# Performance work log

Hardware: AMD Instinct MI355X
Metric: run time of the kernel (lower is better)

Reference implementation:

```python
import jax, jax.numpy as jnp
import numpy as np

B, P, N = 64, 100, 1000
D, H, QD = 128, 8, 16
NUM_PATCHES = 196
NTOT = N + NUM_PATCHES
SQRT_D = float(np.sqrt(D))   # sqrt_embedding_dim
CLIP = 10.0                  # logit_clipping


def setup_inputs() -> dict:
    key = jax.random.key(0)
    ks = jax.random.split(key, 10)
    return {
        "encoded_last_node": jax.random.normal(ks[0], (B, P, D), jnp.float32),
        "ninf_mask": jnp.zeros((B, P, N), jnp.float32),
        "q_first": jax.random.normal(ks[1], (B, H, P, QD), jnp.float32),
        "k": jax.random.normal(ks[2], (B, H, NTOT, QD), jnp.float32),
        "v": jax.random.normal(ks[3], (B, H, NTOT, QD), jnp.float32),
        "single_head_key": jax.random.normal(ks[4], (B, D, N), jnp.float32),
        "Wq_last": jax.random.normal(ks[5], (D, H * QD), jnp.float32) * 0.05,
        "mh_combine": jax.random.normal(ks[6], (H * QD, D), jnp.float32) * 0.05,
        "edge_bias": jax.random.normal(ks[7], (B, N, N), jnp.float32) * 0.1,
        "current_node": jax.random.randint(ks[8], (B, P), 0, N, jnp.int64),
        "num_patches": NUM_PATCHES,
    }


def reference(encoded_last_node, ninf_mask, q_first, k, v, single_head_key,
              Wq_last, mh_combine, edge_bias, current_node, num_patches):
    b, p, _ = encoded_last_node.shape
    h, qd = q_first.shape[1], q_first.shape[3]

    # q_last = reshape_by_heads(F.linear(x, Wq_last_para))  -> [B,H,P,qd]
    q_last = (encoded_last_node @ Wq_last.T).reshape(b, p, h, qd).transpose(0, 2, 1, 3)
    q = q_first + q_last

    # multi-head attention with mask extended by zero columns for patch tokens
    mask_full = jnp.pad(ninf_mask, ((0, 0), (0, 0), (0, num_patches)))  # [B,P,Ntot]
    score = jnp.einsum('bhpd,bhnd->bhpn', q, k) / jnp.sqrt(jnp.float32(qd))
    weights = jax.nn.softmax(score + mask_full[:, None, :, :], axis=-1)
    out = jnp.einsum('bhpn,bhnd->bhpd', weights, v)
    out_concat = out.transpose(0, 2, 1, 3).reshape(b, p, h * qd)  # [B,P,D]

    mh_atten_out = out_concat @ mh_combine.T                       # [B,P,D]

    # pointer-style single-head score with tanh clipping
    score2 = jnp.einsum('bpd,bdn->bpn', mh_atten_out, single_head_key)
    score_clipped = CLIP * jnp.tanh(score2 / SQRT_D)

    # gather edge bias row for current node: bias[b,p,n] = edge_bias[b, current_node[b,p], n]
    bias_row = jnp.take_along_axis(edge_bias, current_node[:, :, None], axis=1)
    probs = jax.nn.softmax(score_clipped + bias_row + ninf_mask, axis=-1)
    return probs
```

## Files before the change

### kernel.cpp

```cpp
#include <hip/hip_runtime.h>
#include <hip/hip_bf16.h>
#include <math.h>

#define BB 64
#define PP 100
#define NN 1000
#define DD 128
#define HH 8
#define QDQ 16
#define NTOT 1196
#define HALFK 598
#define CH 128
#define QROWS 16
#define LOG2E 1.44269504088896f
#define EXP2(x) __builtin_amdgcn_exp2f(x)

typedef float f2 __attribute__((ext_vector_type(2)));
static __device__ __forceinline__ f2 splat2(float v) { f2 r; r.x = v; r.y = v; return r; }
#define PKFMA(a, b, c) __builtin_elementwise_fma((a), (b), (c))

__global__ __launch_bounds__(256) void k_prep(const float* __restrict__ x,
                                              const float* __restrict__ Wq,
                                              const float* __restrict__ qf,
                                              float* __restrict__ qout,
                                              const float* __restrict__ mask,
                                              __hip_bfloat16* __restrict__ mt) {
  __shared__ float sw[128 * 65];
  __shared__ float xs[QROWS * DD];
  int tid = threadIdx.x;

  if (blockIdx.x < 400) {
    int row0 = blockIdx.x * QROWS;
    for (int i = tid; i < QROWS * DD / 4; i += 256)
      ((float4*)xs)[i] = ((const float4*)(x + (size_t)row0 * DD))[i];

    int j = tid & 127, rr = tid >> 7;
    float acc[8];
#pragma unroll
    for (int i = 0; i < 8; ++i) acc[i] = 0.f;

    for (int half = 0; half < 2; ++half) {
      __syncthreads();
      for (int idx = tid; idx < 128 * 64; idx += 256) {
        int jj = idx >> 6, dl = idx & 63;
        sw[jj * 65 + dl] = Wq[jj * DD + half * 64 + dl];
      }
      __syncthreads();
#pragma unroll
      for (int ri = 0; ri < 8; ++ri) {
        int r = 2 * ri + rr;
        float a = acc[ri];
#pragma unroll 16
        for (int dl = 0; dl < 64; ++dl)
          a += xs[r * DD + half * 64 + dl] * sw[j * 65 + dl];
        acc[ri] = a;
      }
    }
#pragma unroll
    for (int ri = 0; ri < 8; ++ri) {
      int bp = row0 + 2 * ri + rr;
      int b = bp / PP, p = bp % PP;
      int h = j >> 4, qd = j & 15;
      size_t qi = ((size_t)(b * HH + h) * PP + p) * QDQ + qd;
      qout[qi] = acc[ri] + qf[qi];
    }
  } else {
    float (*tile)[65] = (float(*)[65])sw;
    int t = blockIdx.x - 400;
    int b = t / 38, rem = t % 38;
    int nt = rem % 19, pt = rem / 19;
    int tx = tid & 63, ty = tid >> 6;
    int n0 = nt * 64, p0 = pt * 64;
#pragma unroll
    for (int r = ty; r < 64; r += 4) {
      int p = p0 + r, n = n0 + tx;
      tile[r][tx] = (p < PP && n < NN) ? mask[((size_t)b * PP + p) * NN + n] * LOG2E - 20.f
                                       : -20.f;
    }
    __syncthreads();
#pragma unroll
    for (int r = ty; r < 64; r += 4) {
      int n = n0 + r, p = p0 + tx;
      int pp = ((p & 63) << 1) | (p >> 6);
      if (n < NTOT)
        mt[((size_t)b * NTOT + n) * 128 + pp] = __float2bfloat16(tile[tx][r]);
    }
  }
}

#define QKDOT(qv, K0, K1, K2, K3) \
  (qv[0] * K0.x + qv[1] * K0.y + qv[2] * K0.z + qv[3] * K0.w \
 + qv[4] * K1.x + qv[5] * K1.y + qv[6] * K1.z + qv[7] * K1.w \
 + qv[8] * K2.x + qv[9] * K2.y + qv[10] * K2.z + qv[11] * K2.w \
 + qv[12] * K3.x + qv[13] * K3.y + qv[14] * K3.z + qv[15] * K3.w)

#define PVADD(av, wt, V0, V1, V2, V3) { \
  av[0] += (wt) * V0.x;  av[1] += (wt) * V0.y;  av[2] += (wt) * V0.z;  av[3] += (wt) * V0.w; \
  av[4] += (wt) * V1.x;  av[5] += (wt) * V1.y;  av[6] += (wt) * V1.z;  av[7] += (wt) * V1.w; \
  av[8] += (wt) * V2.x;  av[9] += (wt) * V2.y;  av[10] += (wt) * V2.z; av[11] += (wt) * V2.w; \
  av[12] += (wt) * V3.x; av[13] += (wt) * V3.y; av[14] += (wt) * V3.z; av[15] += (wt) * V3.w; }

__global__ __launch_bounds__(512) void k_mha(const float* __restrict__ kk,
                                             const float* __restrict__ vv,
                                             const float* __restrict__ qws,
                                             const unsigned int* __restrict__ mt32,
                                             float* __restrict__ part) {
  int bid = blockIdx.x;
  int swz = (bid & 7) * 128 + (bid >> 3);
  int bh = swz >> 1, half = swz & 1;
  int b = bh >> 3;
  int tid = threadIdx.x;
  int w = tid >> 6;
  int lane = tid & 63;
  int p2 = lane + 64;
  int pc2 = p2 < PP ? p2 : PP - 1;

  __shared__ __align__(16) float smem_f[8192];
  float4* s4 = (float4*)smem_f;

  float q1[QDQ], q2[QDQ];
  const float sc0 = 0.25f * LOG2E;
  {
    const float* qrow1 = qws + ((size_t)bh * PP + lane) * QDQ;
    const float* qrow2 = qws + ((size_t)bh * PP + pc2) * QDQ;
#pragma unroll
    for (int jj = 0; jj < QDQ; jj += 4) {
      float4 a4 = *(const float4*)(qrow1 + jj);
      q1[jj] = a4.x * sc0; q1[jj + 1] = a4.y * sc0;
      q1[jj + 2] = a4.z * sc0; q1[jj + 3] = a4.w * sc0;
      float4 b4 = *(const float4*)(qrow2 + jj);
      q2[jj] = b4.x * sc0; q2[jj + 1] = b4.y * sc0;
      q2[jj + 2] = b4.z * sc0; q2[jj + 3] = b4.w * sc0;
    }
  }

  float acc1[QDQ], acc2[QDQ];
#pragma unroll
  for (int jj = 0; jj < QDQ; ++jj) { acc1[jj] = 0.f; acc2[jj] = 0.f; }
  float l1 = 0.f, l2 = 0.f;

  const float4* kg4 = (const float4*)(kk + (size_t)bh * NTOT * QDQ);
  const float4* vg4 = (const float4*)(vv + (size_t)bh * NTOT * QDQ);
  int key0 = half * HALFK;
  int gbase = key0 * 4;
  int lim = NTOT * 4 - 1;

  float4 rk, rv;
  { int gi = gbase + tid; gi = gi < lim ? gi : lim; rk = kg4[gi]; rv = vg4[gi]; }

  int cur = 0;
  for (int c = 0; c < 5; ++c) {
    int base = c * CH;
    int L = HALFK - base; if (L > CH) L = CH;
    __syncthreads();
    s4[cur * 1024 + tid] = rk;
    s4[cur * 1024 + 512 + tid] = rv;
    __syncthreads();
    if (c < 4) {
      int gi = gbase + (c + 1) * 512 + tid; gi = gi < lim ? gi : lim;
      rk = kg4[gi]; rv = vg4[gi];
    }
    const unsigned int* mrow = mt32 + ((size_t)b * NTOT + key0 + base) * 64;
    int kb = cur * 1024, vb = cur * 1024 + 512;

    unsigned int nmm = mrow[w * 64 + lane];
    for (int i = w; i < L; i += 8) {
      unsigned int mm = nmm;
      int inx = i + 8; inx = inx < L ? inx : i;
      nmm = mrow[inx * 64 + lane];

      float4 k0 = s4[kb + i * 4 + 0], k1 = s4[kb + i * 4 + 1];
      float4 k2 = s4[kb + i * 4 + 2], k3 = s4[kb + i * 4 + 3];
      float s1 = QKDOT(q1, k0, k1, k2, k3);
      float s2 = QKDOT(q2, k0, k1, k2, k3);
      float w1 = EXP2(s1 + __uint_as_float(mm << 16));
      float w2 = EXP2(s2 + __uint_as_float(mm & 0xffff0000u));
      l1 += w1; l2 += w2;
      float4 v0 = s4[vb + i * 4 + 0], v1 = s4[vb + i * 4 + 1];
      float4 v2 = s4[vb + i * 4 + 2], v3 = s4[vb + i * 4 + 3];
      PVADD(acc1, w1, v0, v1, v2, v3)
      PVADD(acc2, w2, v0, v1, v2, v3)
    }
    cur ^= 1;
  }

  __syncthreads();
  if (w < 4) {
    float* r = smem_f + ((size_t)w * PP + lane) * 17;
#pragma unroll
    for (int jj = 0; jj < QDQ; ++jj) r[jj] = acc1[jj];
    r[16] = l1;
    if (p2 < PP) {
      float* r2 = smem_f + ((size_t)w * PP + p2) * 17;
#pragma unroll
      for (int jj = 0; jj < QDQ; ++jj) r2[jj] = acc2[jj];
      r2[16] = l2;
    }
  }
  __syncthreads();
  if (w >= 4) {
    float* r = smem_f + ((size_t)(w - 4) * PP + lane) * 17;
#pragma unroll
    for (int jj = 0; jj < QDQ; ++jj) r[jj] += acc1[jj];
    r[16] += l1;
    if (p2 < PP) {
      float* r2 = smem_f + ((size_t)(w - 4) * PP + p2) * 17;
#pragma unroll
      for (int jj = 0; jj < QDQ; ++jj) r2[jj] += acc2[jj];
      r2[16] += l2;
    }
  }
  __syncthreads();
  for (int idx = tid; idx < PP * 17; idx += 512) {
    int pp2 = idx / 17, e = idx % 17;
    float vsum = smem_f[(0 * PP + pp2) * 17 + e] + smem_f[(1 * PP + pp2) * 17 + e]
               + smem_f[(2 * PP + pp2) * 17 + e] + smem_f[(3 * PP + pp2) * 17 + e];
    part[((size_t)swz * PP + pp2) * 17 + e] = vsum;
  }
}

__global__ __launch_bounds__(256) void k_combine(const float* __restrict__ part,
                                                 const float* __restrict__ MC,
                                                 float* __restrict__ mh) {
  __shared__ float sw[128 * 65];
  __shared__ float oc[QROWS * DD];
  int tid = threadIdx.x;
  int row0 = blockIdx.x * QROWS;

  for (int i = tid; i < QROWS * DD; i += 256) {
    int r = i >> 7, t = i & 127;
    int bp = row0 + r, b = bp / PP, p = bp % PP;
    int qd = t & 15, h = t >> 4;
    int bh = b * HH + h;
    const float* r0 = part + (((size_t)(bh * 2 + 0)) * PP + p) * 17;
    const float* r1 = part + (((size_t)(bh * 2 + 1)) * PP + p) * 17;
    float A = r0[qd] + r1[qd];
    float L = r0[16] + r1[16];
    oc[i] = A / L;
  }

  int j = tid & 127, rr = tid >> 7;
  float acc[8];
#pragma unroll
  for (int i = 0; i < 8; ++i) acc[i] = 0.f;

  for (int half = 0; half < 2; ++half) {
    __syncthreads();
    for (int idx = tid; idx < 128 * 64; idx += 256) {
      int jj = idx >> 6, dl = idx & 63;
      sw[jj * 65 + dl] = MC[jj * DD + half * 64 + dl];
    }
    __syncthreads();
#pragma unroll
    for (int ri = 0; ri < 8; ++ri) {
      int r = 2 * ri + rr;
      float a = acc[ri];
#pragma unroll 16
      for (int dl = 0; dl < 64; ++dl)
        a += oc[r * DD + half * 64 + dl] * sw[j * 65 + dl];
      acc[ri] = a;
    }
  }
#pragma unroll
  for (int ri = 0; ri < 8; ++ri) {
    int bp = row0 + 2 * ri + rr;
    mh[(size_t)bp * DD + j] = acc[ri];
  }
}

__global__ __launch_bounds__(256) void k_score2(const float* __restrict__ mh,
                                                const float* __restrict__ shk,
                                                float* __restrict__ sc) {
  int bid = blockIdx.x;
  int swz = (bid & 7) * 128 + (bid >> 3);
  int b = swz >> 4, nt = swz & 15;
  int tid = threadIdx.x; int nl = tid & 31, pg = tid >> 5;
  __shared__ float A[PP * 132];
  for (int idx = tid; idx < PP * DD; idx += 256)
    A[(idx >> 7) * 132 + (idx & 127)] = mh[(size_t)b * PP * DD + idx];
  __syncthreads();

  int na = nt * 64 + nl, nb2 = na + 32;
  int nca = na < NN ? na : NN - 1, ncb = nb2 < NN ? nb2 : NN - 1;
  const float* S = shk + (size_t)b * DD * NN;
  f2 accv[13];
#pragma unroll
  for (int i = 0; i < 13; ++i) accv[i] = splat2(0.f);

  for (int d = 0; d < DD; d += 4) {
    f2 s0, s1, s2, s3;
    s0.x = S[(size_t)(d + 0) * NN + nca]; s0.y = S[(size_t)(d + 0) * NN + ncb];
    s1.x = S[(size_t)(d + 1) * NN + nca]; s1.y = S[(size_t)(d + 1) * NN + ncb];
    s2.x = S[(size_t)(d + 2) * NN + nca]; s2.y = S[(size_t)(d + 2) * NN + ncb];
    s3.x = S[(size_t)(d + 3) * NN + nca]; s3.y = S[(size_t)(d + 3) * NN + ncb];
#pragma unroll
    for (int i = 0; i < 13; ++i) {
      int p = pg + (i << 3);
      if (p < PP) {
        const float4 a4 = *(const float4*)&A[p * 132 + d];
        accv[i] = PKFMA(splat2(a4.x), s0, accv[i]);
        accv[i] = PKFMA(splat2(a4.y), s1, accv[i]);
        accv[i] = PKFMA(splat2(a4.z), s2, accv[i]);
        accv[i] = PKFMA(splat2(a4.w), s3, accv[i]);
      }
    }
  }
#pragma unroll
  for (int i = 0; i < 13; ++i) {
    int p = pg + (i << 3);
    if (p < PP) {
      size_t base = ((size_t)b * PP + p) * NN;
      if (na < NN) sc[base + na] = accv[i].x;
      if (nb2 < NN) sc[base + nb2] = accv[i].y;
    }
  }
}

__global__ __launch_bounds__(256) void k_finsm(const float* __restrict__ sc,
                                               const float* __restrict__ eb,
                                               const int* __restrict__ cn,
                                               const float* __restrict__ mask,
                                               float* __restrict__ out) {
  int bid = blockIdx.x;
  int bp = (bid & 7) * 800 + (bid >> 3);
  int b = bp / PP;
  int t = threadIdx.x;
  int node = cn[bp];
  const float* scp = sc + (size_t)bp * NN;
  const float* ebp = eb + ((size_t)b * NN + node) * NN;
  const float* mp = mask + (size_t)bp * NN;
  const float inv_sqrtD = 0.08838834764831845f;

  float vals[4];
  float s = 0.f;
#pragma unroll
  for (int i = 0; i < 4; ++i) {
    int n = t + (i << 8);
    if (n < NN) {
      float z = scp[n] * inv_sqrtD;
      float e = EXP2(2.f * LOG2E * z);
      float th10 = 10.f - 20.f * __builtin_amdgcn_rcpf(e + 1.f);
      float lg = th10 + ebp[n] + mp[n];
      float e2 = EXP2(lg * LOG2E);
      vals[i] = e2;
      s += e2;
    } else {
      vals[i] = 0.f;
    }
  }
#pragma unroll
  for (int off = 32; off; off >>= 1) s += __shfl_xor(s, off);
  __shared__ float red[4];
  int w = t >> 6, lane = t & 63;
  if (lane == 0) red[w] = s;
  __syncthreads();
  s = (red[0] + red[1]) + (red[2] + red[3]);
  float inv = 1.f / s;
#pragma unroll
  for (int i = 0; i < 4; ++i) {
    int n = t + (i << 8);
    if (n < NN) out[(size_t)bp * NN + n] = vals[i] * inv;
  }
}

extern "C" void kernel_launch(void* const* d_in, const int* in_sizes, int n_in,
                              void* d_out, int out_size, void* d_ws, size_t ws_size,
                              hipStream_t stream) {
  const float* x    = (const float*)d_in[0];
  const float* mask = (const float*)d_in[1];
  const float* qf   = (const float*)d_in[2];
  const float* kk   = (const float*)d_in[3];
  const float* vv   = (const float*)d_in[4];
  const float* shk  = (const float*)d_in[5];
  const float* Wq   = (const float*)d_in[6];
  const float* MC   = (const float*)d_in[7];
  const float* eb   = (const float*)d_in[8];
  const int*   cn   = (const int*)d_in[9];

  float* out = (float*)d_out;
  float* ws = (float*)d_ws;
  float* q_ws = ws;
  float* part = ws + 819200;
  float* mh   = ws + 2560000;
  float* reg  = ws + 3379200;
  __hip_bfloat16* mt = (__hip_bfloat16*)reg;
  float* sc   = reg;

  hipLaunchKernelGGL(k_prep, dim3(2832), dim3(256), 0, stream, x, Wq, qf, q_ws, mask, mt);
  hipLaunchKernelGGL(k_mha, dim3(1024), dim3(512), 0, stream, kk, vv, q_ws,
                     (const unsigned int*)mt, part);
  hipLaunchKernelGGL(k_combine, dim3(400), dim3(256), 0, stream, part, MC, mh);
  hipLaunchKernelGGL(k_score2, dim3(1024), dim3(256), 0, stream, mh, shk, sc);
  hipLaunchKernelGGL(k_finsm, dim3(6400), dim3(256), 0, stream, sc, eb, cn, mask, out);
}
```

Baseline: 219.9 us.

## Move attention QK and PV onto bf16 MFMA with split-precision hi/lo operands

Replaces the scalar FP32 dot-product attention loop in k_mha with 32x32x16 bf16 MFMA instructions. Q, K, V and the softmax weights are each split into a bf16 high part and a bf16 residual, and three MFMAs per product recover near-FP32 accuracy. The mask is pre-laid out per query row, padded to 1280 keys, and loaded directly as the MFMA accumulator initializer. The block size drops to 256 threads and k_prep gets more blocks for the new mask layout. This trades scalar VALU FMA work for matrix-core throughput, at the cost of extra conversion and shuffle work, LDS transposes, and a larger mask buffer.

```diff
diff --git a/kernel.cpp b/kernel.cpp
--- a/kernel.cpp
+++ b/kernel.cpp
@@ -1,5 +1,4 @@
 #include <hip/hip_runtime.h>
-#include <hip/hip_bf16.h>
 #include <math.h>
 
 #define BB 64
@@ -9,22 +8,31 @@
 #define HH 8
 #define QDQ 16
 #define NTOT 1196
-#define HALFK 598
-#define CH 128
 #define QROWS 16
 #define LOG2E 1.44269504088896f
 #define EXP2(x) __builtin_amdgcn_exp2f(x)
 
 typedef float f2 __attribute__((ext_vector_type(2)));
+typedef short s8v __attribute__((ext_vector_type(8)));
+typedef float f16v __attribute__((ext_vector_type(16)));
+
 static __device__ __forceinline__ f2 splat2(float v) { f2 r; r.x = v; r.y = v; return r; }
 #define PKFMA(a, b, c) __builtin_elementwise_fma((a), (b), (c))
+
+static __device__ __forceinline__ unsigned pkhi(float a, float b) {
+  return (__float_as_uint(a) >> 16) | (__float_as_uint(b) & 0xffff0000u);
+}
+static __device__ __forceinline__ float truncbf(float a) {
+  return __uint_as_float(__float_as_uint(a) & 0xffff0000u);
+}
+#define MFMA32(a, b, c) __builtin_amdgcn_mfma_f32_32x32x16_bf16((a), (b), (c), 0, 0, 0)
 
 __global__ __launch_bounds__(256) void k_prep(const float* __restrict__ x,
                                               const float* __restrict__ Wq,
                                               const float* __restrict__ qf,
                                               float* __restrict__ qout,
                                               const float* __restrict__ mask,
-                                              __hip_bfloat16* __restrict__ mt) {
+                                              unsigned short* __restrict__ m2) {
   __shared__ float sw[128 * 65];
   __shared__ float xs[QROWS * DD];
   int tid = threadIdx.x;
@@ -65,157 +73,198 @@
       qout[qi] = acc[ri] + qf[qi];
     }
   } else {
-    float (*tile)[65] = (float(*)[65])sw;
-    int t = blockIdx.x - 400;
-    int b = t / 38, rem = t % 38;
-    int nt = rem % 19, pt = rem / 19;
-    int tx = tid & 63, ty = tid >> 6;
-    int n0 = nt * 64, p0 = pt * 64;
-#pragma unroll
-    for (int r = ty; r < 64; r += 4) {
-      int p = p0 + r, n = n0 + tx;
-      tile[r][tx] = (p < PP && n < NN) ? mask[((size_t)b * PP + p) * NN + n] * LOG2E - 20.f
-                                       : -20.f;
-    }
-    __syncthreads();
-#pragma unroll
-    for (int r = ty; r < 64; r += 4) {
-      int n = n0 + r, p = p0 + tx;
-      int pp = ((p & 63) << 1) | (p >> 6);
-      if (n < NTOT)
-        mt[((size_t)b * NTOT + n) * 128 + pp] = __float2bfloat16(tile[tx][r]);
-    }
-  }
-}
-
-#define QKDOT(qv, K0, K1, K2, K3) \
-  (qv[0] * K0.x + qv[1] * K0.y + qv[2] * K0.z + qv[3] * K0.w \
- + qv[4] * K1.x + qv[5] * K1.y + qv[6] * K1.z + qv[7] * K1.w \
- + qv[8] * K2.x + qv[9] * K2.y + qv[10] * K2.z + qv[11] * K2.w \
- + qv[12] * K3.x + qv[13] * K3.y + qv[14] * K3.z + qv[15] * K3.w)
-
-#define PVADD(av, wt, V0, V1, V2, V3) { \
-  av[0] += (wt) * V0.x;  av[1] += (wt) * V0.y;  av[2] += (wt) * V0.z;  av[3] += (wt) * V0.w; \
-  av[4] += (wt) * V1.x;  av[5] += (wt) * V1.y;  av[6] += (wt) * V1.z;  av[7] += (wt) * V1.w; \
-  av[8] += (wt) * V2.x;  av[9] += (wt) * V2.y;  av[10] += (wt) * V2.z; av[11] += (wt) * V2.w; \
-  av[12] += (wt) * V3.x; av[13] += (wt) * V3.y; av[14] += (wt) * V3.z; av[15] += (wt) * V3.w; }
-
-__global__ __launch_bounds__(512) void k_mha(const float* __restrict__ kk,
+    int t2 = blockIdx.x - 400;
+    int b = t2 >> 7, q = t2 & 127;
+    unsigned short* dst = m2 + (size_t)(b * 128 + q) * 1280;
+    const float* srow = mask + ((size_t)b * PP + (q < PP ? q : PP - 1)) * NN;
+    for (int j = tid; j < 1280; j += 256) {
+      int h = j >= 640 ? 1 : 0;
+      int jj = j - h * 640;
+      float val;
+      if (q >= PP || jj >= 598) {
+        val = -1e4f;
+      } else {
+        int n = h * 598 + jj;
+        val = (n < NN) ? srow[n] * LOG2E - 20.f : -20.f;
+      }
+      dst[j] = (unsigned short)(__float_as_uint(val) >> 16);
+    }
+  }
+}
+
+__global__ __launch_bounds__(256) void k_mha(const float* __restrict__ kk,
                                              const float* __restrict__ vv,
                                              const float* __restrict__ qws,
-                                             const unsigned int* __restrict__ mt32,
+                                             const unsigned short* __restrict__ m2,
                                              float* __restrict__ part) {
   int bid = blockIdx.x;
   int swz = (bid & 7) * 128 + (bid >> 3);
   int bh = swz >> 1, half = swz & 1;
   int b = bh >> 3;
   int tid = threadIdx.x;
-  int w = tid >> 6;
-  int lane = tid & 63;
-  int p2 = lane + 64;
-  int pc2 = p2 < PP ? p2 : PP - 1;
-
-  __shared__ __align__(16) float smem_f[8192];
-  float4* s4 = (float4*)smem_f;
-
-  float q1[QDQ], q2[QDQ];
-  const float sc0 = 0.25f * LOG2E;
+  int w = tid >> 6, lane = tid & 63;
+  int L = lane >> 5, ln = lane & 31;
+  bool lo = (L == 0);
+
+  __shared__ __align__(16) char pool[27264];
+  char* KspB = pool;
+  char* VThB = pool + 8192;
+  char* VTlB = pool + 12288;
+  char* QhB  = pool + 16384;
+  char* QlB  = pool + 20480;
+
   {
-    const float* qrow1 = qws + ((size_t)bh * PP + lane) * QDQ;
-    const float* qrow2 = qws + ((size_t)bh * PP + pc2) * QDQ;
-#pragma unroll
-    for (int jj = 0; jj < QDQ; jj += 4) {
-      float4 a4 = *(const float4*)(qrow1 + jj);
-      q1[jj] = a4.x * sc0; q1[jj + 1] = a4.y * sc0;
-      q1[jj + 2] = a4.z * sc0; q1[jj + 3] = a4.w * sc0;
-      float4 b4 = *(const float4*)(qrow2 + jj);
-      q2[jj] = b4.x * sc0; q2[jj + 1] = b4.y * sc0;
-      q2[jj + 2] = b4.z * sc0; q2[jj + 3] = b4.w * sc0;
-    }
-  }
-
-  float acc1[QDQ], acc2[QDQ];
-#pragma unroll
-  for (int jj = 0; jj < QDQ; ++jj) { acc1[jj] = 0.f; acc2[jj] = 0.f; }
-  float l1 = 0.f, l2 = 0.f;
-
-  const float4* kg4 = (const float4*)(kk + (size_t)bh * NTOT * QDQ);
-  const float4* vg4 = (const float4*)(vv + (size_t)bh * NTOT * QDQ);
-  int key0 = half * HALFK;
-  int gbase = key0 * 4;
-  int lim = NTOT * 4 - 1;
-
-  float4 rk, rv;
-  { int gi = gbase + tid; gi = gi < lim ? gi : lim; rk = kg4[gi]; rv = vg4[gi]; }
-
-  int cur = 0;
+    const float* qrow = qws + (size_t)bh * (PP * QDQ);
+    for (int i = tid; i < 128 * 16; i += 256) {
+      int p = i >> 4, qd = i & 15;
+      float v = (p < PP) ? qrow[p * QDQ + qd] * (0.25f * LOG2E) : 0.f;
+      ((unsigned short*)QhB)[i] = (unsigned short)(__float_as_uint(v) >> 16);
+      float rl = v - truncbf(v);
+      ((unsigned short*)QlB)[i] = (unsigned short)(__float_as_uint(rl) >> 16);
+    }
+  }
+
+  const float4* kf4 = (const float4*)kk + (size_t)bh * NTOT * 4;
+  const float4* vf4 = (const float4*)vv + (size_t)bh * NTOT * 4;
+
+  f16v Oacc[4];
+  float lacc[4];
+#pragma unroll
+  for (int qt = 0; qt < 4; ++qt) {
+    lacc[qt] = 0.f;
+#pragma unroll
+    for (int r = 0; r < 16; ++r) Oacc[qt][r] = 0.f;
+  }
+  s8v QhF[4], QlF[4];
+
   for (int c = 0; c < 5; ++c) {
-    int base = c * CH;
-    int L = HALFK - base; if (L > CH) L = CH;
     __syncthreads();
-    s4[cur * 1024 + tid] = rk;
-    s4[cur * 1024 + 512 + tid] = rv;
+#pragma unroll
+    for (int rep = 0; rep < 2; ++rep) {
+      int f = tid + rep * 256;
+      int key_l = f >> 2, qd0 = (f & 3) << 2;
+      int j = c * 128 + key_l;
+      int jc = j < 598 ? j : 597;
+      size_t gidx = (size_t)(half * 598 + jc) * 4 + (qd0 >> 2);
+      float4 k4 = kf4[gidx];
+      unsigned kh01 = pkhi(k4.x, k4.y), kh23 = pkhi(k4.z, k4.w);
+      float r0 = k4.x - truncbf(k4.x), r1 = k4.y - truncbf(k4.y);
+      float r2 = k4.z - truncbf(k4.z), r3 = k4.w - truncbf(k4.w);
+      unsigned kl01 = pkhi(r0, r1), kl23 = pkhi(r2, r3);
+      *(uint2*)(KspB + key_l * 64 + qd0 * 2) = make_uint2(kh01, kh23);
+      *(uint2*)(KspB + key_l * 64 + 32 + qd0 * 2) = make_uint2(kl01, kl23);
+      float4 v4 = vf4[gidx];
+      float ve0 = v4.x, ve1 = v4.y, ve2 = v4.z, ve3 = v4.w;
+      ((unsigned short*)VThB)[(qd0 + 0) * 128 + key_l] = (unsigned short)(__float_as_uint(ve0) >> 16);
+      ((unsigned short*)VThB)[(qd0 + 1) * 128 + key_l] = (unsigned short)(__float_as_uint(ve1) >> 16);
+      ((unsigned short*)VThB)[(qd0 + 2) * 128 + key_l] = (unsigned short)(__float_as_uint(ve2) >> 16);
+      ((unsigned short*)VThB)[(qd0 + 3) * 128 + key_l] = (unsigned short)(__float_as_uint(ve3) >> 16);
+      float w0 = ve0 - truncbf(ve0), w1 = ve1 - truncbf(ve1);
+      float w2 = ve2 - truncbf(ve2), w3 = ve3 - truncbf(ve3);
+      ((unsigned short*)VTlB)[(qd0 + 0) * 128 + key_l] = (unsigned short)(__float_as_uint(w0) >> 16);
+      ((unsigned short*)VTlB)[(qd0 + 1) * 128 + key_l] = (unsigned short)(__float_as_uint(w1) >> 16);
+      ((unsigned short*)VTlB)[(qd0 + 2) * 128 + key_l] = (unsigned short)(__float_as_uint(w2) >> 16);
+      ((unsigned short*)VTlB)[(qd0 + 3) * 128 + key_l] = (unsigned short)(__float_as_uint(w3) >> 16);
+    }
     __syncthreads();
-    if (c < 4) {
-      int gi = gbase + (c + 1) * 512 + tid; gi = gi < lim ? gi : lim;
-      rk = kg4[gi]; rv = vg4[gi];
-    }
-    const unsigned int* mrow = mt32 + ((size_t)b * NTOT + key0 + base) * 64;
-    int kb = cur * 1024, vb = cur * 1024 + 512;
-
-    unsigned int nmm = mrow[w * 64 + lane];
-    for (int i = w; i < L; i += 8) {
-      unsigned int mm = nmm;
-      int inx = i + 8; inx = inx < L ? inx : i;
-      nmm = mrow[inx * 64 + lane];
-
-      float4 k0 = s4[kb + i * 4 + 0], k1 = s4[kb + i * 4 + 1];
-      float4 k2 = s4[kb + i * 4 + 2], k3 = s4[kb + i * 4 + 3];
-      float s1 = QKDOT(q1, k0, k1, k2, k3);
-      float s2 = QKDOT(q2, k0, k1, k2, k3);
-      float w1 = EXP2(s1 + __uint_as_float(mm << 16));
-      float w2 = EXP2(s2 + __uint_as_float(mm & 0xffff0000u));
-      l1 += w1; l2 += w2;
-      float4 v0 = s4[vb + i * 4 + 0], v1 = s4[vb + i * 4 + 1];
-      float4 v2 = s4[vb + i * 4 + 2], v3 = s4[vb + i * 4 + 3];
-      PVADD(acc1, w1, v0, v1, v2, v3)
-      PVADD(acc2, w2, v0, v1, v2, v3)
-    }
-    cur ^= 1;
-  }
+    if (c == 0) {
+#pragma unroll
+      for (int qt = 0; qt < 4; ++qt) {
+        int qr = qt * 32 + ln;
+        QhF[qt] = *(const s8v*)(QhB + qr * 32 + L * 16);
+        QlF[qt] = *(const s8v*)(QlB + qr * 32 + L * 16);
+      }
+    }
+    int ktb = w * 32;
+    s8v KhF = *(const s8v*)(KspB + (ktb + ln) * 64 + L * 16);
+    s8v KlF = *(const s8v*)(KspB + (ktb + ln) * 64 + 32 + L * 16);
+    int vr = ln & 15;
+    s8v VhS0 = *(const s8v*)(VThB + vr * 256 + (ktb + L * 8) * 2);
+    s8v VhS1 = *(const s8v*)(VThB + vr * 256 + (ktb + 16 + L * 8) * 2);
+    s8v VlS0 = *(const s8v*)(VTlB + vr * 256 + (ktb + L * 8) * 2);
+    s8v VlS1 = *(const s8v*)(VTlB + vr * 256 + (ktb + 16 + L * 8) * 2);
+    size_t mkey = (size_t)half * 640 + c * 128 + ktb + 4 * L;
+#pragma unroll
+    for (int qt = 0; qt < 4; ++qt) {
+      const unsigned short* mrow = m2 + (size_t)(b * 128 + qt * 32 + ln) * 1280 + mkey;
+      f16v acc;
+#pragma unroll
+      for (int g = 0; g < 4; ++g) {
+        uint2 md = *(const uint2*)(mrow + g * 8);
+        acc[g * 4 + 0] = __uint_as_float(md.x << 16);
+        acc[g * 4 + 1] = __uint_as_float(md.x & 0xffff0000u);
+        acc[g * 4 + 2] = __uint_as_float(md.y << 16);
+        acc[g * 4 + 3] = __uint_as_float(md.y & 0xffff0000u);
+      }
+      acc = MFMA32(KhF, QhF[qt], acc);
+      acc = MFMA32(KhF, QlF[qt], acc);
+      acc = MFMA32(KlF, QhF[qt], acc);
+      float p[16];
+      float ls = 0.f;
+#pragma unroll
+      for (int r = 0; r < 16; ++r) { p[r] = EXP2(acc[r]); ls += p[r]; }
+      lacc[qt] += ls;
+#pragma unroll
+      for (int s = 0; s < 2; ++s) {
+        unsigned a0 = pkhi(p[8 * s + 0], p[8 * s + 1]), a1 = pkhi(p[8 * s + 2], p[8 * s + 3]);
+        unsigned b0 = pkhi(p[8 * s + 4], p[8 * s + 5]), b1 = pkhi(p[8 * s + 6], p[8 * s + 7]);
+        unsigned sa0 = __shfl_xor(a0, 32), sa1 = __shfl_xor(a1, 32);
+        unsigned sb0 = __shfl_xor(b0, 32), sb1 = __shfl_xor(b1, 32);
+        uint4 phu = make_uint4(lo ? a0 : sb0, lo ? a1 : sb1, lo ? sa0 : b0, lo ? sa1 : b1);
+        float t0 = p[8 * s + 0] - truncbf(p[8 * s + 0]), t1 = p[8 * s + 1] - truncbf(p[8 * s + 1]);
+        float t2 = p[8 * s + 2] - truncbf(p[8 * s + 2]), t3 = p[8 * s + 3] - truncbf(p[8 * s + 3]);
+        float t4 = p[8 * s + 4] - truncbf(p[8 * s + 4]), t5 = p[8 * s + 5] - truncbf(p[8 * s + 5]);
+        float t6 = p[8 * s + 6] - truncbf(p[8 * s + 6]), t7 = p[8 * s + 7] - truncbf(p[8 * s + 7]);
+        unsigned c0 = pkhi(t0, t1), c1 = pkhi(t2, t3);
+        unsigned e0 = pkhi(t4, t5), e1 = pkhi(t6, t7);
+        unsigned sc0 = __shfl_xor(c0, 32), sc1 = __shfl_xor(c1, 32);
+        unsigned se0 = __shfl_xor(e0, 32), se1 = __shfl_xor(e1, 32);
+        uint4 plu = make_uint4(lo ? c0 : se0, lo ? c1 : se1, lo ? sc0 : e0, lo ? sc1 : e1);
+        s8v APh = *(s8v*)&phu;
+        s8v APl = *(s8v*)&plu;
+        s8v Vh = s ? VhS1 : VhS0;
+        s8v Vl = s ? VlS1 : VlS0;
+        Oacc[qt] = MFMA32(APh, Vh, Oacc[qt]);
+        Oacc[qt] = MFMA32(APh, Vl, Oacc[qt]);
+        Oacc[qt] = MFMA32(APl, Vh, Oacc[qt]);
+      }
+    }
+  }
+
+  float lf[4];
+#pragma unroll
+  for (int qt = 0; qt < 4; ++qt) lf[qt] = lacc[qt] + __shfl_xor(lacc[qt], 32);
 
   __syncthreads();
-  if (w < 4) {
-    float* r = smem_f + ((size_t)w * PP + lane) * 17;
-#pragma unroll
-    for (int jj = 0; jj < QDQ; ++jj) r[jj] = acc1[jj];
-    r[16] = l1;
-    if (p2 < PP) {
-      float* r2 = smem_f + ((size_t)w * PP + p2) * 17;
-#pragma unroll
-      for (int jj = 0; jj < QDQ; ++jj) r2[jj] = acc2[jj];
-      r2[16] = l2;
+  float* marea = (float*)pool;
+  float* larea = (float*)(pool + 25600);
+  if (ln < 16) {
+#pragma unroll
+    for (int qt = 0; qt < 4; ++qt) {
+#pragma unroll
+      for (int r = 0; r < 16; ++r) {
+        int q = qt * 32 + (r & 3) + 8 * (r >> 2) + 4 * L;
+        if (q < PP) marea[(w * PP + q) * 16 + ln] = Oacc[qt][r];
+      }
+    }
+  }
+  if (lane < 32) {
+#pragma unroll
+    for (int qt = 0; qt < 4; ++qt) {
+      int q = qt * 32 + ln;
+      if (q < PP) larea[w * PP + q] = lf[qt];
     }
   }
   __syncthreads();
-  if (w >= 4) {
-    float* r = smem_f + ((size_t)(w - 4) * PP + lane) * 17;
-#pragma unroll
-    for (int jj = 0; jj < QDQ; ++jj) r[jj] += acc1[jj];
-    r[16] += l1;
-    if (p2 < PP) {
-      float* r2 = smem_f + ((size_t)(w - 4) * PP + p2) * 17;
-#pragma unroll
-      for (int jj = 0; jj < QDQ; ++jj) r2[jj] += acc2[jj];
-      r2[16] += l2;
-    }
-  }
-  __syncthreads();
-  for (int idx = tid; idx < PP * 17; idx += 512) {
-    int pp2 = idx / 17, e = idx % 17;
-    float vsum = smem_f[(0 * PP + pp2) * 17 + e] + smem_f[(1 * PP + pp2) * 17 + e]
-               + smem_f[(2 * PP + pp2) * 17 + e] + smem_f[(3 * PP + pp2) * 17 + e];
-    part[((size_t)swz * PP + pp2) * 17 + e] = vsum;
+  for (int idx = tid; idx < PP * 17; idx += 256) {
+    int q = idx / 17, e = idx % 17;
+    float sv;
+    if (e < 16)
+      sv = marea[(0 * PP + q) * 16 + e] + marea[(1 * PP + q) * 16 + e]
+         + marea[(2 * PP + q) * 16 + e] + marea[(3 * PP + q) * 16 + e];
+    else
+      sv = larea[0 * PP + q] + larea[1 * PP + q] + larea[2 * PP + q] + larea[3 * PP + q];
+    part[((size_t)swz * PP + q) * 17 + e] = sv;
   }
 }
 
@@ -383,12 +432,11 @@
   float* part = ws + 819200;
   float* mh   = ws + 2560000;
   float* reg  = ws + 3379200;
-  __hip_bfloat16* mt = (__hip_bfloat16*)reg;
+  unsigned short* m2 = (unsigned short*)reg;
   float* sc   = reg;
 
-  hipLaunchKernelGGL(k_prep, dim3(2832), dim3(256), 0, stream, x, Wq, qf, q_ws, mask, mt);
-  hipLaunchKernelGGL(k_mha, dim3(1024), dim3(512), 0, stream, kk, vv, q_ws,
-                     (const unsigned int*)mt, part);
+  hipLaunchKernelGGL(k_prep, dim3(8592), dim3(256), 0, stream, x, Wq, qf, q_ws, mask, m2);
+  hipLaunchKernelGGL(k_mha, dim3(1024), dim3(256), 0, stream, kk, vv, q_ws, m2, part);
   hipLaunchKernelGGL(k_combine, dim3(400), dim3(256), 0, stream, part, MC, mh);
   hipLaunchKernelGGL(k_score2, dim3(1024), dim3(256), 0, stream, mh, shk, sc);
   hipLaunchKernelGGL(k_finsm, dim3(6400), dim3(256), 0, stream, sc, eb, cn, mask, out);
```

Measured after the change: 200.0 us. 9.1% less time.
